# Optimization experiments

Measured on AMD Instinct MI355X. Metric: run time of the kernel, lower is better.

The kernel has to match this reference:

```python
import jax, jax.numpy as jnp
import numpy as np

B, S, D, H = 4, 2048, 256, 4
HD = D // H          # head_dim = 64
SPARSITY = 0.1
NH2 = H * H          # 16, distill feature size


def _linear_params(key, out_d, in_d):
    # torch nn.Linear default init: U(-1/sqrt(in), 1/sqrt(in)) for W and b
    limit = 1.0 / np.sqrt(in_d)
    kw, kb = jax.random.split(key)
    W = jax.random.uniform(kw, (out_d, in_d), minval=-limit, maxval=limit, dtype=jnp.float32)
    b = jax.random.uniform(kb, (out_d,), minval=-limit, maxval=limit, dtype=jnp.float32)
    return W, b


def setup_inputs() -> dict:
    key = jax.random.key(0)
    ks = jax.random.split(key, 8)
    x = jax.random.normal(ks[0], (B, S, D), dtype=jnp.float32)
    Wq, bq = _linear_params(ks[1], D, D)
    Wk, bk = _linear_params(ks[2], D, D)
    Wv, bv = _linear_params(ks[3], D, D)
    Wd, bd = _linear_params(ks[4], NH2, NH2)      # distill: 16 -> 16
    Wg, bg = _linear_params(ks[5], NH2, D)        # gate: dim -> 16 (then sigmoid)
    Wgp, bgp = _linear_params(ks[6], D, NH2)      # gate_projection: 16 -> dim
    Wo, bo = _linear_params(ks[7], D, D)          # out: dim -> dim
    return dict(x=x, Wq=Wq, bq=bq, Wk=Wk, bk=bk, Wv=Wv, bv=bv,
                Wd=Wd, bd=bd, Wg=Wg, bg=bg, Wgp=Wgp, bgp=bgp, Wo=Wo, bo=bo)


def reference(x, Wq, bq, Wk, bk, Wv, bv, Wd, bd, Wg, bg, Wgp, bgp, Wo, bo):
    b, s, d = x.shape
    scale = HD ** -0.5
    # QKV projections, split into heads: [b, h, s, hd]
    Q = (x @ Wq.T + bq).reshape(b, s, H, HD).transpose(0, 2, 1, 3)
    K = (x @ Wk.T + bk).reshape(b, s, H, HD).transpose(0, 2, 1, 3)
    V = (x @ Wv.T + bv).reshape(b, s, H, HD).transpose(0, 2, 1, 3)
    scores = jnp.einsum('bhqd,bhkd->bhqk', Q, K) * scale  # [b,h,s,s]
    # per-row quantile threshold (torch.quantile linear interpolation == jnp default)
    q = 1.0 - SPARSITY  # 0.9
    thr = jnp.quantile(scores, q, axis=-1, keepdims=True)
    masked = jnp.where(scores >= thr, scores, -jnp.inf)
    probs = jax.nn.softmax(masked, axis=-1)
    att = jnp.einsum('bhqk,bhkd->bhqd', probs, V)
    att = att.transpose(0, 2, 1, 3).reshape(b, s, d)  # [b,s,dim]
    # distill: view as (-1, 16) -> Linear(16,16) -> view back
    distilled = (att.reshape(-1, NH2) @ Wd.T + bd).reshape(b, s, d)
    # gate from mean-pooled input
    g = jax.nn.sigmoid(x.mean(axis=1) @ Wg.T + bg)  # [b,16]
    g = (g @ Wgp.T + bgp)[:, None, :]               # [b,1,dim] broadcast over seq
    mixed = g * distilled + (1.0 - g) * att
    return mixed @ Wo.T + bo
```

## Files before the change

### kernel.cpp

```cpp
#include <hip/hip_runtime.h>
#include <hip/hip_bf16.h>
#include <math.h>


#define CAP 128

typedef __attribute__((ext_vector_type(8))) short short8;
typedef __attribute__((ext_vector_type(4))) float floatx4;
typedef _Float16 half8 __attribute__((ext_vector_type(8)));
typedef _Float16 half4v __attribute__((ext_vector_type(4)));
#define MFMA16(a,b,c) __builtin_amdgcn_mfma_f32_16x16x32_bf16(a,b,c,0,0,0)
#define MFMAH(a,b,c)  __builtin_amdgcn_mfma_f32_16x16x32_f16(a,b,c,0,0,0)

__device__ __forceinline__ float umt(unsigned u){
  return __uint_as_float((u & 0x80000000u) ? (u & 0x7fffffffu) : ~u);
}
__device__ __forceinline__ float wmin_f(float v){
  #pragma unroll
  for (int m=1;m<64;m<<=1) v = fminf(v, __shfl_xor(v,m,64));
  return v;
}
__device__ __forceinline__ int mbcnt64(unsigned long long m){
  return (int)__builtin_amdgcn_mbcnt_hi((unsigned)(m>>32),
         __builtin_amdgcn_mbcnt_lo((unsigned)(m & 0xffffffffull), 0u));
}
__device__ __forceinline__ short8 ldb8(const __hip_bfloat16* p){
  return *(const short8*)p;
}

#define FULLSEL(SU, PSTART, V206, V205)                                        \
  {                                                                            \
    unsigned v = (PSTART);                                                     \
    _Pragma("unroll 1")                                                        \
    for (int bit = 19; bit >= 0; --bit){                                       \
      const float cf = umt(v | (1u << bit));                                   \
      int n = 0;                                                               \
      _Pragma("unroll")                                                        \
      for (int i = 0; i < 32; i++) n += (int)__popcll(__ballot(SU[i] >= cf));  \
      if (n >= 206) v |= (1u << bit);                                          \
    }                                                                          \
    V206 = umt(v);                                                             \
    int cgt = 0; float mn = 3.0e38f;                                           \
    _Pragma("unroll")                                                          \
    for (int i = 0; i < 32; i++){                                              \
      const float u = SU[i];                                                   \
      const bool gt = (u > V206);                                              \
      cgt += (int)__popcll(__ballot(gt));                                      \
      mn = (gt && u < mn) ? u : mn;                                            \
    }                                                                          \
    mn = wmin_f(mn);                                                           \
    V205 = (cgt == 205) ? mn : V206;                                           \
  }

__global__ void xpart_kernel(const float* __restrict__ x, float* __restrict__ xpart,
                             __hip_bfloat16* __restrict__ xh, __hip_bfloat16* __restrict__ xl){
  const int ch = blockIdx.x, b = blockIdx.y, t = threadIdx.x;
  const size_t base = ((size_t)b*2048 + (size_t)ch*16)*256 + t;
  float s = 0.f;
  #pragma unroll
  for (int i=0;i<16;i++){
    const float v = x[base + (size_t)i*256];
    s += v;
    const __hip_bfloat16 h = __float2bfloat16(v);
    xh[base + (size_t)i*256] = h;
    xl[base + (size_t)i*256] = __float2bfloat16(v - __bfloat162float(h));
  }
  xpart[(size_t)(b*128+ch)*256 + t] = s;
}

__global__ void wconv_kernel(const float* __restrict__ Wq, const float* __restrict__ Wk,
                             const float* __restrict__ Wv, const float* __restrict__ Wo,
                             __hip_bfloat16* __restrict__ wh, __hip_bfloat16* __restrict__ wl){
  const int mat = blockIdx.x >> 6;
  const float* W = (mat==0) ? Wq : (mat==1) ? Wk : (mat==2) ? Wv : Wo;
  const int off = (blockIdx.x & 63)*1024 + threadIdx.x*4;
  const float4 v = *(const float4*)&W[off];
  const float vv[4] = {v.x, v.y, v.z, v.w};
  short hs[4], ls[4];
  #pragma unroll
  for (int i=0;i<4;i++){
    const __hip_bfloat16 h = __float2bfloat16(vv[i]);
    const __hip_bfloat16 l = __float2bfloat16(vv[i] - __bfloat162float(h));
    hs[i] = *(const short*)&h; ls[i] = *(const short*)&l;
  }
  const size_t o = (size_t)mat*65536 + off;
  *(short4*)((short*)wh + o) = make_short4(hs[0],hs[1],hs[2],hs[3]);
  *(short4*)((short*)wl + o) = make_short4(ls[0],ls[1],ls[2],ls[3]);
}

__global__ void gate_kernel(const float* __restrict__ xpart,
                            const float* __restrict__ Wg, const float* __restrict__ bg,
                            const float* __restrict__ Wgp,const float* __restrict__ bgp,
                            float* __restrict__ gate_ws){
  __shared__ float xm[256];
  __shared__ float part[16][17];
  __shared__ float g16[16];
  const int t = threadIdx.x;
  const int b = blockIdx.x;
  float s = 0.f;
  for (int ch=0; ch<128; ch++) s += xpart[(size_t)(b*128+ch)*256 + t];
  xm[t] = s * (1.0f/2048.0f);
  __syncthreads();
  {
    const int j = t >> 4, dg = t & 15;
    float p = 0.f;
    #pragma unroll
    for (int d=0; d<16; d++) p = fmaf(xm[dg*16+d], Wg[j*256 + dg*16 + d], p);
    part[j][dg] = p;
  }
  __syncthreads();
  if (t < 16){
    float z = bg[t];
    #pragma unroll
    for (int g=0; g<16; g++) z += part[t][g];
    g16[t] = 1.0f/(1.0f + __expf(-z));
  }
  __syncthreads();
  float z2 = bgp[t];
  #pragma unroll
  for (int j=0;j<16;j++) z2 = fmaf(g16[j], Wgp[t*16+j], z2);
  gate_ws[b*256 + t] = z2;
}

__global__ __launch_bounds__(256) void qkv_gemm(
    const __hip_bfloat16* __restrict__ xh, const __hip_bfloat16* __restrict__ xl,
    const __hip_bfloat16* __restrict__ wh, const __hip_bfloat16* __restrict__ wl,
    const float* __restrict__ bq, const float* __restrict__ bk, const float* __restrict__ bv,
    __hip_bfloat16* __restrict__ qh, __hip_bfloat16* __restrict__ ql,
    __hip_bfloat16* __restrict__ kh, __hip_bfloat16* __restrict__ kl,
    _Float16* __restrict__ vth, _Float16* __restrict__ vtl){
  __shared__ short Ah[64][40], Al[64][40];
  __shared__ short Bh[64][40], Bl[64][40];
  const int m0 = blockIdx.x * 64;
  const int n0g = blockIdx.y * 64;
  const int sect = n0g >> 8;
  const int nl0 = n0g & 255;
  const __hip_bfloat16* Wh = wh + (size_t)sect*65536;
  const __hip_bfloat16* Wl = wl + (size_t)sect*65536;
  const float* bias = (sect==0) ? bq : ((sect==1) ? bk : bv);
  const int tid = threadIdx.x;
  const int lr = tid >> 2, lc = tid & 3;
  const int w = tid >> 6, ln = tid & 63;
  const int lm = ln & 15, lk = (ln >> 4) * 8;

  floatx4 acc[4];
  #pragma unroll
  for (int tl=0;tl<4;tl++) acc[tl] = (floatx4){0.f,0.f,0.f,0.f};

  for (int k0 = 0; k0 < 256; k0 += 32){
    const short8 a_h = ldb8(xh + (size_t)(m0 +lr)*256 + k0 + lc*8);
    const short8 a_l = ldb8(xl + (size_t)(m0 +lr)*256 + k0 + lc*8);
    const short8 b_h = ldb8(Wh + (size_t)(nl0+lr)*256 + k0 + lc*8);
    const short8 b_l = ldb8(Wl + (size_t)(nl0+lr)*256 + k0 + lc*8);
    __syncthreads();
    *(short8*)&Ah[lr][lc*8] = a_h;
    *(short8*)&Al[lr][lc*8] = a_l;
    *(short8*)&Bh[lr][lc*8] = b_h;
    *(short8*)&Bl[lr][lc*8] = b_l;
    __syncthreads();
    const short8 ah8 = *(const short8*)&Ah[w*16+lm][lk];
    const short8 al8 = *(const short8*)&Al[w*16+lm][lk];
    #pragma unroll
    for (int tl = 0; tl < 4; tl++){
      const short8 bh8 = *(const short8*)&Bh[tl*16+lm][lk];
      const short8 bl8 = *(const short8*)&Bl[tl*16+lm][lk];
      acc[tl] = MFMA16(ah8, bh8, acc[tl]);
      acc[tl] = MFMA16(al8, bh8, acc[tl]);
      acc[tl] = MFMA16(ah8, bl8, acc[tl]);
      acc[tl] = MFMA16(al8, bl8, acc[tl]);
    }
  }

  #pragma unroll
  for (int tl = 0; tl < 4; tl++){
    const int f = nl0 + tl*16 + lm;
    const int hh = f >> 6, hd = f & 63;
    const float bf = bias[f];
    if (sect == 2){
      const int mB = m0 + w*16 + (ln >> 4)*4;
      const int bidx = mB >> 11, s0 = mB & 2047;
      half4v hv, lv;
      #pragma unroll
      for (int i=0;i<4;i++){
        const float val = acc[tl][i] + bf;
        const _Float16 hx = (_Float16)val;
        hv[i] = hx;
        lv[i] = (_Float16)(val - (float)hx);
      }
      const size_t row = (size_t)((bidx*4+hh)*64 + hd);
      *(half4v*)(vth + row*2048 + s0) = hv;
      *(half4v*)(vtl + row*2048 + s0) = lv;
    } else {
      #pragma unroll
      for (int i=0;i<4;i++){
        const int m = m0 + w*16 + (ln >> 4)*4 + i;
        const int bidx = m >> 11, s = m & 2047;
        const float val = acc[tl][i] + bf;
        const size_t idx = (size_t)((bidx*4+hh)*2048 + s)*64 + hd;
        const __hip_bfloat16 hi = __float2bfloat16(val);
        const float lo = val - __bfloat162float(hi);
        if (sect == 0){ qh[idx] = hi; ql[idx] = __float2bfloat16(lo); }
        else          { kh[idx] = hi; kl[idx] = __float2bfloat16(lo); }
      }
    }
  }
}

__global__ __launch_bounds__(512, 4) void attn_kernel(
    const __hip_bfloat16* __restrict__ qh, const __hip_bfloat16* __restrict__ ql,
    const __hip_bfloat16* __restrict__ kh, const __hip_bfloat16* __restrict__ kl,
    const _Float16* __restrict__ vth, const _Float16* __restrict__ vtl,
    const float* __restrict__ Wd, const float* __restrict__ bd,
    const float* __restrict__ gate_ws,
    __hip_bfloat16* __restrict__ mixh, __hip_bfloat16* __restrict__ mixl){
  __shared__ __align__(16) char smem[70336];
  float (*buf0)[516] = (float (*)[516])smem;
  float (*buf1)[516] = (float (*)[516])(smem + 33024);
  float (*obuf)[66] = (float (*)[66])(smem + 66048);
  float* zbuf = (float*)(smem + 70272);

  const int bh = blockIdx.y;
  const int q0 = blockIdx.x * 16;
  const int tid = threadIdx.x;
  const int w = tid >> 6, ln = tid & 63;
  const int lm = ln & 15;
  const int lk = (ln >> 4) * 8;
  const int qa = 2*w, qb = 2*w + 1;

  const __hip_bfloat16* Qh = qh + ((size_t)bh*2048 + q0)*64;
  const __hip_bfloat16* Ql = ql + ((size_t)bh*2048 + q0)*64;
  const __hip_bfloat16* Kh = kh + ((size_t)bh*2048 + w*256)*64;
  const __hip_bfloat16* Kl = kl + ((size_t)bh*2048 + w*256)*64;

  float su0[32], su1[32];

  const short8 ah0 = ldb8(Qh + lm*64 + lk);
  const short8 ah1 = ldb8(Qh + lm*64 + 32 + lk);
  const short8 al0 = ldb8(Ql + lm*64 + lk);
  const short8 al1 = ldb8(Ql + lm*64 + 32 + lk);

  #pragma unroll
  for (int c = 0; c < 4; c++){
    float (*bufc)[516] = (c & 1) ? buf1 : buf0;
    floatx4 acc[4];
    #pragma unroll
    for (int tl = 0; tl < 4; tl++){
      const int krow = c*64 + tl*16 + lm;
      short8 bh0 = ldb8(Kh + krow*64 + lk);
      short8 bh1 = ldb8(Kh + krow*64 + 32 + lk);
      short8 bl0 = ldb8(Kl + krow*64 + lk);
      short8 bl1 = ldb8(Kl + krow*64 + 32 + lk);
      floatx4 a = {0.f,0.f,0.f,0.f};
      a = MFMA16(ah0, bh0, a);
      a = MFMA16(ah1, bh1, a);
      a = MFMA16(al0, bh0, a);
      a = MFMA16(al1, bh1, a);
      a = MFMA16(ah0, bl0, a);
      a = MFMA16(ah1, bl1, a);
      a = MFMA16(al0, bl0, a);
      a = MFMA16(al1, bl1, a);
      acc[tl] = a;
    }
    const int wr = (ln >> 4) * 4;
    #pragma unroll
    for (int tl = 0; tl < 4; tl++){
      const int col = w*64 + tl*16 + lm;
      bufc[wr+0][col] = acc[tl].x * 0.125f;
      bufc[wr+1][col] = acc[tl].y * 0.125f;
      bufc[wr+2][col] = acc[tl].z * 0.125f;
      bufc[wr+3][col] = acc[tl].w * 0.125f;
    }
    __syncthreads();
    float4 ra0 = *(const float4*)&bufc[qa][4*ln];
    float4 ra1 = *(const float4*)&bufc[qa][256 + 4*ln];
    float4 rb0 = *(const float4*)&bufc[qb][4*ln];
    float4 rb1 = *(const float4*)&bufc[qb][256 + 4*ln];
    const int o = c*8;
    su0[o+0]=ra0.x; su0[o+1]=ra0.y; su0[o+2]=ra0.z; su0[o+3]=ra0.w;
    su0[o+4]=ra1.x; su0[o+5]=ra1.y; su0[o+6]=ra1.z; su0[o+7]=ra1.w;
    su1[o+0]=rb0.x; su1[o+1]=rb0.y; su1[o+2]=rb0.z; su1[o+3]=rb0.w;
    su1[o+4]=rb1.x; su1[o+5]=rb1.y; su1[o+6]=rb1.z; su1[o+7]=rb1.w;
  }
  __syncthreads();

  unsigned p0 = 0, p1 = 0;
  #pragma unroll 1
  for (int bit = 31; bit >= 20; --bit){
    const float c0f = umt(p0 | (1u << bit));
    const float c1f = umt(p1 | (1u << bit));
    int v0 = 0, n1 = 0;
    #pragma unroll
    for (int i = 0; i < 32; i++){
      v0 += (su0[i] >= c0f) ? 1 : 0;
      n1 += (int)__popcll(__ballot(su1[i] >= c1f));
    }
    #pragma unroll
    for (int m=1;m<64;m<<=1) v0 += __shfl_xor(v0,m,64);
    p0 |= (v0 >= 206) ? (1u << bit) : 0u;
    if (n1 >= 206) p1 |= (1u << bit);
  }

  const int b = bh >> 2, h = bh & 3;

  const float pf0  = umt(p0),             pf1  = umt(p1);
  const float hif0 = umt(p0 + 0x100000u), hif1 = umt(p1 + 0x100000u);
  float* cand0 = (float*)(smem + 33024 + (size_t)w*1024);
  float* cand1 = (float*)(smem + 33024 + (size_t)w*1024 + 512);

  int above0 = 0, nc0 = 0, above1 = 0, nc1 = 0;
  float mx0 = -3.0e38f, mx1 = -3.0e38f, mnab0 = 3.0e38f, mnab1 = 3.0e38f;
  #pragma unroll
  for (int i = 0; i < 32; i++){
    const float u0 = su0[i], u1 = su1[i];
    mx0 = fmaxf(mx0, u0);
    mx1 = fmaxf(mx1, u1);
    const bool ab0 = (u0 >= hif0), ab1 = (u1 >= hif1);
    above0 += ab0 ? 1 : 0;
    above1 += ab1 ? 1 : 0;
    if (ab0) mnab0 = fminf(mnab0, u0);
    if (ab1) mnab1 = fminf(mnab1, u1);
    const bool cd0 = (u0 >= pf0) && !ab0, cd1 = (u1 >= pf1) && !ab1;
    const unsigned long long bal0 = __ballot(cd0);
    if (cd0){
      const int pos = nc0 + mbcnt64(bal0);
      if (pos < CAP) cand0[pos] = u0;
    }
    nc0 += (int)__popcll(bal0);
    const unsigned long long bal1 = __ballot(cd1);
    if (cd1){
      const int pos = nc1 + mbcnt64(bal1);
      if (pos < CAP) cand1[pos] = u1;
    }
    nc1 += (int)__popcll(bal1);
  }
  int ab01 = above0 | (above1 << 16);
  #pragma unroll
  for (int m=1;m<64;m<<=1){
    ab01  += __shfl_xor(ab01, m,64);
    mx0   = fmaxf(mx0,   __shfl_xor(mx0,  m,64));
    mx1   = fmaxf(mx1,   __shfl_xor(mx1,  m,64));
    mnab0 = fminf(mnab0, __shfl_xor(mnab0,m,64));
    mnab1 = fminf(mnab1, __shfl_xor(mnab1,m,64));
  }
  above0 = ab01 & 0xffff;
  above1 = ab01 >> 16;

  float v206_0, v205_0, v206_1, v205_1;
  if (__builtin_expect(nc0 <= CAP && nc1 <= CAP, 1)){
    const int j0 = 206 - above0, j1 = 206 - above1;
    const float cv00 = (ln      < nc0) ? cand0[ln]      : -3.0e38f;
    const float cv01 = (ln + 64 < nc0) ? cand0[ln + 64] : -3.0e38f;
    const float cv10 = (ln      < nc1) ? cand1[ln]      : -3.0e38f;
    const float cv11 = (ln + 64 < nc1) ? cand1[ln + 64] : -3.0e38f;
    unsigned v0 = p0, v1 = p1;
    #pragma unroll 1
    for (int bit = 19; bit >= 0; --bit){
      const float cf0 = umt(v0 | (1u << bit));
      const float cf1 = umt(v1 | (1u << bit));
      const int n0 = (int)__popcll(__ballot(cv00 >= cf0))
                   + (int)__popcll(__ballot(cv01 >= cf0));
      const int n1 = (int)__popcll(__ballot(cv10 >= cf1))
                   + (int)__popcll(__ballot(cv11 >= cf1));
      if (n0 >= j0) v0 |= (1u << bit);
      if (n1 >= j1) v1 |= (1u << bit);
    }
    v206_0 = umt(v0);
    v206_1 = umt(v1);
    const int cgtc0 = (int)__popcll(__ballot(cv00 > v206_0))
                    + (int)__popcll(__ballot(cv01 > v206_0));
    const int cgtc1 = (int)__popcll(__ballot(cv10 > v206_1))
                    + (int)__popcll(__ballot(cv11 > v206_1));
    float mnc0 = 3.0e38f, mnc1 = 3.0e38f;
    if (cv00 > v206_0) mnc0 = fminf(mnc0, cv00);
    if (cv01 > v206_0) mnc0 = fminf(mnc0, cv01);
    if (cv10 > v206_1) mnc1 = fminf(mnc1, cv10);
    if (cv11 > v206_1) mnc1 = fminf(mnc1, cv11);
    #pragma unroll
    for (int m=1;m<64;m<<=1){
      mnc0 = fminf(mnc0, __shfl_xor(mnc0,m,64));
      mnc1 = fminf(mnc1, __shfl_xor(mnc1,m,64));
    }
    const int cgt0 = above0 + cgtc0, cgt1 = above1 + cgtc1;
    v205_0 = (cgt0 == 205) ? ((cgtc0 > 0) ? mnc0 : mnab0) : v206_0;
    v205_1 = (cgt1 == 205) ? ((cgtc1 > 0) ? mnc1 : mnab1) : v206_1;
  } else {
    FULLSEL(su0, p0, v206_0, v205_0);
    FULLSEL(su1, p1, v206_1, v205_1);
  }

  const float thr0 = (float)((double)v206_0 + 0.3*((double)v205_0 - (double)v206_0));
  const float thr1 = (float)((double)v206_1 + 0.3*((double)v205_1 - (double)v206_1));

  float zl0 = 0.f, zl1 = 0.f;
  char* rba = smem + (size_t)qa*2048 + ((size_t)(ln >> 4) << 9)
            + (size_t)((((ln & 15) << 3)) ^ ((qa & 7) << 4));
  char* rbb = smem + (size_t)qb*2048 + ((size_t)(ln >> 4) << 9)
            + (size_t)((((ln & 15) << 3)) ^ ((qb & 7) << 4));

  const int ct = w & 3, khq = w >> 2;
  const int arow = ln & 15;
  const int sw = (arow & 7) << 4;
  const char* prow = smem + (size_t)arow*2048;
  const int klog0 = (khq << 10) + ((ln >> 4) << 4);
  floatx4 acch = {0.f,0.f,0.f,0.f};
  floatx4 accl = {0.f,0.f,0.f,0.f};

  #pragma unroll
  for (int hp = 0; hp < 2; hp++){
    #pragma unroll
    for (int c = 0; c < 4; c++){
      half4v pk0, pk1;
      #pragma unroll
      for (int jj = 0; jj < 4; jj++){
        const int i = c*8 + hp*4 + jj;
        const float s0 = su0[i], s1 = su1[i];
        const float pr0 = (s0 >= thr0) ? __expf(s0 - mx0) : 0.f;
        const float pr1 = (s1 >= thr1) ? __expf(s1 - mx1) : 0.f;
        const _Float16 ph0 = (_Float16)pr0;
        const _Float16 ph1 = (_Float16)pr1;
        zl0 += (float)ph0;
        zl1 += (float)ph1;
        pk0[jj] = ph0;
        pk1[jj] = ph1;
      }
      *(half4v*)(rba + c*128) = pk0;
      *(half4v*)(rbb + c*128) = pk1;
    }
    if (hp == 1){
      #pragma unroll
      for (int m=1;m<64;m<<=1){
        zl0 += __shfl_xor(zl0,m,64);
        zl1 += __shfl_xor(zl1,m,64);
      }
      if (ln == 0){ zbuf[qa] = 1.0f / zl0; zbuf[qb] = 1.0f / zl1; }
    }
    __syncthreads();

    const _Float16* vhp_ = vth + ((size_t)bh*64 + ct*16 + arow)*2048
                         + (hp << 10) + (khq << 9) + ((ln >> 4) << 3);
    const _Float16* vlp_ = vtl + ((size_t)bh*64 + ct*16 + arow)*2048
                         + (hp << 10) + (khq << 9) + ((ln >> 4) << 3);
    #pragma unroll 4
    for (int kk = 0; kk < 16; kk++){
      const half8 a   = *(const half8*)(prow + ((klog0 + kk*64) ^ sw));
      const half8 vh8 = *(const half8*)(vhp_ + kk*32);
      const half8 vl8 = *(const half8*)(vlp_ + kk*32);
      acch = MFMAH(a, vh8, acch);
      accl = MFMAH(a, vl8, accl);
    }
    if (hp == 0) __syncthreads();
  }
  floatx4 acc = acch + accl;

  float gt = 0.f, bda = 0.f;
  float wdv[16];
  if (khq == 1){
    const int r0 = (ln >> 4) * 4;
    #pragma unroll
    for (int i = 0; i < 4; i++) obuf[r0+i][ct*16 + arow] = acc[i];
  } else {
    gt  = gate_ws[(size_t)b*256 + h*64 + ct*16 + arow];
    bda = bd[arow];
    #pragma unroll
    for (int m4 = 0; m4 < 4; m4++){
      const float4 t4 = *(const float4*)&Wd[arow*16 + m4*4];
      wdv[m4*4+0]=t4.x; wdv[m4*4+1]=t4.y; wdv[m4*4+2]=t4.z; wdv[m4*4+3]=t4.w;
    }
  }
  __syncthreads();
  if (khq == 0){
    const int r0 = (ln >> 4) * 4;
    const int gb = ln & 48;
    #pragma unroll
    for (int i = 0; i < 4; i++){
      const int r = r0 + i;
      const float o = (acc[i] + obuf[r][ct*16 + arow]) * zbuf[r];
      float d = bda;
      #pragma unroll
      for (int m = 0; m < 16; m++)
        d = fmaf(__shfl(o, gb + m, 64), wdv[m], d);
      const float mixed = gt*d + (1.0f - gt)*o;
      const size_t oidx = (size_t)(b*2048 + q0 + r)*256 + h*64 + ct*16 + arow;
      const __hip_bfloat16 mhv = __float2bfloat16(mixed);
      mixh[oidx] = mhv;
      mixl[oidx] = __float2bfloat16(mixed - __bfloat162float(mhv));
    }
  }
}

__global__ __launch_bounds__(256) void out_gemm(
    const __hip_bfloat16* __restrict__ mh, const __hip_bfloat16* __restrict__ ml,
    const __hip_bfloat16* __restrict__ wh, const __hip_bfloat16* __restrict__ wl,
    const float* __restrict__ bo, float* __restrict__ out){
  __shared__ short Ah[64][40], Al[64][40];
  __shared__ short Bh[64][40], Bl[64][40];
  const int m0 = blockIdx.x * 64;
  const int n0 = blockIdx.y * 64;
  const __hip_bfloat16* Wh = wh + (size_t)3*65536;
  const __hip_bfloat16* Wl = wl + (size_t)3*65536;
  const int tid = threadIdx.x;
  const int lr = tid >> 2, lc = tid & 3;
  const int w = tid >> 6, ln = tid & 63;
  const int lm = ln & 15, lk = (ln >> 4) * 8;

  floatx4 acc[4];
  #pragma unroll
  for (int tl=0;tl<4;tl++) acc[tl] = (floatx4){0.f,0.f,0.f,0.f};

  for (int k0 = 0; k0 < 256; k0 += 32){
    const short8 a_h = ldb8(mh + (size_t)(m0+lr)*256 + k0 + lc*8);
    const short8 a_l = ldb8(ml + (size_t)(m0+lr)*256 + k0 + lc*8);
    const short8 b_h = ldb8(Wh + (size_t)(n0+lr)*256 + k0 + lc*8);
    const short8 b_l = ldb8(Wl + (size_t)(n0+lr)*256 + k0 + lc*8);
    __syncthreads();
    *(short8*)&Ah[lr][lc*8] = a_h;
    *(short8*)&Al[lr][lc*8] = a_l;
    *(short8*)&Bh[lr][lc*8] = b_h;
    *(short8*)&Bl[lr][lc*8] = b_l;
    __syncthreads();
    const short8 ah8 = *(const short8*)&Ah[w*16+lm][lk];
    const short8 al8 = *(const short8*)&Al[w*16+lm][lk];
    #pragma unroll
    for (int tl = 0; tl < 4; tl++){
      const short8 bh8 = *(const short8*)&Bh[tl*16+lm][lk];
      const short8 bl8 = *(const short8*)&Bl[tl*16+lm][lk];
      acc[tl] = MFMA16(ah8, bh8, acc[tl]);
      acc[tl] = MFMA16(al8, bh8, acc[tl]);
      acc[tl] = MFMA16(ah8, bl8, acc[tl]);
      acc[tl] = MFMA16(al8, bl8, acc[tl]);
    }
  }

  #pragma unroll
  for (int tl = 0; tl < 4; tl++){
    const int f = n0 + tl*16 + lm;
    const float bf = bo[f];
    #pragma unroll
    for (int i=0;i<4;i++){
      const int m = m0 + w*16 + (ln >> 4)*4 + i;
      out[(size_t)m*256 + f] = acc[tl][i] + bf;
    }
  }
}

extern "C" void kernel_launch(void* const* d_in, const int* in_sizes, int n_in,
                              void* d_out, int out_size, void* d_ws, size_t ws_size,
                              hipStream_t stream) {
  const float* x   = (const float*)d_in[0];
  const float* Wq  = (const float*)d_in[1];  const float* bq  = (const float*)d_in[2];
  const float* Wk  = (const float*)d_in[3];  const float* bk  = (const float*)d_in[4];
  const float* Wv  = (const float*)d_in[5];  const float* bv  = (const float*)d_in[6];
  const float* Wd  = (const float*)d_in[7];  const float* bd  = (const float*)d_in[8];
  const float* Wg  = (const float*)d_in[9];  const float* bg  = (const float*)d_in[10];
  const float* Wgp = (const float*)d_in[11]; const float* bgp = (const float*)d_in[12];
  const float* Wo  = (const float*)d_in[13]; const float* bo  = (const float*)d_in[14];

  char* base = (char*)d_ws;
  __hip_bfloat16* mixh = (__hip_bfloat16*)(base);
  __hip_bfloat16* mixl = (__hip_bfloat16*)(base + (size_t)( 4<<20));
  __hip_bfloat16* qh = (__hip_bfloat16*)(base + (size_t)( 8<<20));
  __hip_bfloat16* ql = (__hip_bfloat16*)(base + (size_t)(12<<20));
  __hip_bfloat16* kh = (__hip_bfloat16*)(base + (size_t)(16<<20));
  __hip_bfloat16* kl = (__hip_bfloat16*)(base + (size_t)(20<<20));
  _Float16* vth = (_Float16*)(base + (size_t)(24<<20));
  _Float16* vtl = (_Float16*)(base + (size_t)(28<<20));
  __hip_bfloat16* xh = (__hip_bfloat16*)(base + (size_t)(32<<20));
  __hip_bfloat16* xl = (__hip_bfloat16*)(base + (size_t)(36<<20));
  __hip_bfloat16* wh = (__hip_bfloat16*)(base + (size_t)(40<<20));
  __hip_bfloat16* wl = (__hip_bfloat16*)(base + (size_t)(40<<20) + (512<<10));
  float* xpart  = (float*)(base + (size_t)(41<<20));
  float* gate_ws= (float*)(base + (size_t)(41<<20) + (512<<10));

  xpart_kernel<<<dim3(128,4), 256, 0, stream>>>(x, xpart, xh, xl);
  wconv_kernel<<<256, 256, 0, stream>>>(Wq, Wk, Wv, Wo, wh, wl);
  gate_kernel<<<4, 256, 0, stream>>>(xpart, Wg, bg, Wgp, bgp, gate_ws);
  qkv_gemm<<<dim3(128,12), 256, 0, stream>>>(xh, xl, wh, wl, bq, bk, bv,
                                             qh, ql, kh, kl, vth, vtl);
  attn_kernel<<<dim3(128,16), 512, 0, stream>>>(qh, ql, kh, kl, vth, vtl,
                                                Wd, bd, gate_ws, mixh, mixl);
  out_gemm<<<dim3(128,4), 256, 0, stream>>>(mixh, mixl, wh, wl, bo, (float*)d_out);
}
```

Before: 397.0 us.

## Bracket quantile candidates with mean/std window instead of 12-bit radix prefix

Replaces the 12-iteration radix prefix pass over all 2048 scores per row with a single mean/variance reduction, then keeps candidates in the window [mean+sd, mean+1.5sd) for the exact bitwise selection. The candidate cap doubles to 256 and the fine selection now scans all 32 bits over four registers per lane. If the window does not bracket the 206th value or overflows, it falls back to a full 32-bit radix select over every score. This relies on near-Gaussian score distributions; heavy-tailed rows would take the slower fallback more often.

After: 380.8 us. 4.1% less time.

```diff
diff --git a/kernel.cpp b/kernel.cpp
--- a/kernel.cpp
+++ b/kernel.cpp
@@ -3,7 +3,7 @@
 #include <math.h>
 
 
-#define CAP 128
+#define CAP 256
 
 typedef __attribute__((ext_vector_type(8))) short short8;
 typedef __attribute__((ext_vector_type(4))) float floatx4;
@@ -28,11 +28,11 @@
   return *(const short8*)p;
 }
 
-#define FULLSEL(SU, PSTART, V206, V205)                                        \
+#define FULLSEL(SU, V206, V205)                                                \
   {                                                                            \
-    unsigned v = (PSTART);                                                     \
+    unsigned v = 0u;                                                           \
     _Pragma("unroll 1")                                                        \
-    for (int bit = 19; bit >= 0; --bit){                                       \
+    for (int bit = 31; bit >= 0; --bit){                                       \
       const float cf = umt(v | (1u << bit));                                   \
       int n = 0;                                                               \
       _Pragma("unroll")                                                        \
@@ -283,43 +283,44 @@
   }
   __syncthreads();
 
-  unsigned p0 = 0, p1 = 0;
-  #pragma unroll 1
-  for (int bit = 31; bit >= 20; --bit){
-    const float c0f = umt(p0 | (1u << bit));
-    const float c1f = umt(p1 | (1u << bit));
-    int v0 = 0, n1 = 0;
-    #pragma unroll
-    for (int i = 0; i < 32; i++){
-      v0 += (su0[i] >= c0f) ? 1 : 0;
-      n1 += (int)__popcll(__ballot(su1[i] >= c1f));
-    }
-    #pragma unroll
-    for (int m=1;m<64;m<<=1) v0 += __shfl_xor(v0,m,64);
-    p0 |= (v0 >= 206) ? (1u << bit) : 0u;
-    if (n1 >= 206) p1 |= (1u << bit);
-  }
-
-  const int b = bh >> 2, h = bh & 3;
-
-  const float pf0  = umt(p0),             pf1  = umt(p1);
-  const float hif0 = umt(p0 + 0x100000u), hif1 = umt(p1 + 0x100000u);
-  float* cand0 = (float*)(smem + 33024 + (size_t)w*1024);
-  float* cand1 = (float*)(smem + 33024 + (size_t)w*1024 + 512);
-
-  int above0 = 0, nc0 = 0, above1 = 0, nc1 = 0;
-  float mx0 = -3.0e38f, mx1 = -3.0e38f, mnab0 = 3.0e38f, mnab1 = 3.0e38f;
+  float sm0 = 0.f, sm1 = 0.f, sq0 = 0.f, sq1 = 0.f;
+  float mx0 = -3.0e38f, mx1 = -3.0e38f;
   #pragma unroll
   for (int i = 0; i < 32; i++){
     const float u0 = su0[i], u1 = su1[i];
-    mx0 = fmaxf(mx0, u0);
-    mx1 = fmaxf(mx1, u1);
-    const bool ab0 = (u0 >= hif0), ab1 = (u1 >= hif1);
+    sm0 += u0; sm1 += u1;
+    sq0 = fmaf(u0, u0, sq0); sq1 = fmaf(u1, u1, sq1);
+    mx0 = fmaxf(mx0, u0); mx1 = fmaxf(mx1, u1);
+  }
+  #pragma unroll
+  for (int m=1;m<64;m<<=1){
+    sm0 += __shfl_xor(sm0,m,64); sm1 += __shfl_xor(sm1,m,64);
+    sq0 += __shfl_xor(sq0,m,64); sq1 += __shfl_xor(sq1,m,64);
+    mx0 = fmaxf(mx0, __shfl_xor(mx0,m,64));
+    mx1 = fmaxf(mx1, __shfl_xor(mx1,m,64));
+  }
+  const float mean0 = sm0 * (1.f/2048.f), mean1 = sm1 * (1.f/2048.f);
+  const float sd0 = sqrtf(fmaxf(sq0*(1.f/2048.f) - mean0*mean0, 0.f));
+  const float sd1 = sqrtf(fmaxf(sq1*(1.f/2048.f) - mean1*mean1, 0.f));
+  const float lo0 = mean0 + sd0, lo1 = mean1 + sd1;
+  const float hi0 = fmaf(1.5f, sd0, mean0), hi1 = fmaf(1.5f, sd1, mean1);
+
+  const int b = bh >> 2, h = bh & 3;
+
+  float* cand0 = (float*)(smem + 33024 + (size_t)w*2048);
+  float* cand1 = (float*)(smem + 33024 + (size_t)w*2048 + 1024);
+
+  int above0 = 0, nc0 = 0, above1 = 0, nc1 = 0;
+  float mnab0 = 3.0e38f, mnab1 = 3.0e38f;
+  #pragma unroll
+  for (int i = 0; i < 32; i++){
+    const float u0 = su0[i], u1 = su1[i];
+    const bool ab0 = (u0 >= hi0), ab1 = (u1 >= hi1);
     above0 += ab0 ? 1 : 0;
     above1 += ab1 ? 1 : 0;
     if (ab0) mnab0 = fminf(mnab0, u0);
     if (ab1) mnab1 = fminf(mnab1, u1);
-    const bool cd0 = (u0 >= pf0) && !ab0, cd1 = (u1 >= pf1) && !ab1;
+    const bool cd0 = (u0 >= lo0) && !ab0, cd1 = (u1 >= lo1) && !ab1;
     const unsigned long long bal0 = __ballot(cd0);
     if (cd0){
       const int pos = nc0 + mbcnt64(bal0);
@@ -337,44 +338,61 @@
   #pragma unroll
   for (int m=1;m<64;m<<=1){
     ab01  += __shfl_xor(ab01, m,64);
-    mx0   = fmaxf(mx0,   __shfl_xor(mx0,  m,64));
-    mx1   = fmaxf(mx1,   __shfl_xor(mx1,  m,64));
     mnab0 = fminf(mnab0, __shfl_xor(mnab0,m,64));
     mnab1 = fminf(mnab1, __shfl_xor(mnab1,m,64));
   }
   above0 = ab01 & 0xffff;
   above1 = ab01 >> 16;
 
+  const bool vld0 = (above0 < 206) && (above0 + nc0 >= 206) && (nc0 <= CAP);
+  const bool vld1 = (above1 < 206) && (above1 + nc1 >= 206) && (nc1 <= CAP);
+
   float v206_0, v205_0, v206_1, v205_1;
-  if (__builtin_expect(nc0 <= CAP && nc1 <= CAP, 1)){
+  if (__builtin_expect(vld0 && vld1, 1)){
     const int j0 = 206 - above0, j1 = 206 - above1;
-    const float cv00 = (ln      < nc0) ? cand0[ln]      : -3.0e38f;
-    const float cv01 = (ln + 64 < nc0) ? cand0[ln + 64] : -3.0e38f;
-    const float cv10 = (ln      < nc1) ? cand1[ln]      : -3.0e38f;
-    const float cv11 = (ln + 64 < nc1) ? cand1[ln + 64] : -3.0e38f;
-    unsigned v0 = p0, v1 = p1;
+    const float cv00 = (ln       < nc0) ? cand0[ln]       : -3.0e38f;
+    const float cv01 = (ln + 64  < nc0) ? cand0[ln + 64]  : -3.0e38f;
+    const float cv02 = (ln + 128 < nc0) ? cand0[ln + 128] : -3.0e38f;
+    const float cv03 = (ln + 192 < nc0) ? cand0[ln + 192] : -3.0e38f;
+    const float cv10 = (ln       < nc1) ? cand1[ln]       : -3.0e38f;
+    const float cv11 = (ln + 64  < nc1) ? cand1[ln + 64]  : -3.0e38f;
+    const float cv12 = (ln + 128 < nc1) ? cand1[ln + 128] : -3.0e38f;
+    const float cv13 = (ln + 192 < nc1) ? cand1[ln + 192] : -3.0e38f;
+    unsigned v0 = 0u, v1 = 0u;
     #pragma unroll 1
-    for (int bit = 19; bit >= 0; --bit){
+    for (int bit = 31; bit >= 0; --bit){
       const float cf0 = umt(v0 | (1u << bit));
       const float cf1 = umt(v1 | (1u << bit));
       const int n0 = (int)__popcll(__ballot(cv00 >= cf0))
-                   + (int)__popcll(__ballot(cv01 >= cf0));
+                   + (int)__popcll(__ballot(cv01 >= cf0))
+                   + (int)__popcll(__ballot(cv02 >= cf0))
+                   + (int)__popcll(__ballot(cv03 >= cf0));
       const int n1 = (int)__popcll(__ballot(cv10 >= cf1))
-                   + (int)__popcll(__ballot(cv11 >= cf1));
+                   + (int)__popcll(__ballot(cv11 >= cf1))
+                   + (int)__popcll(__ballot(cv12 >= cf1))
+                   + (int)__popcll(__ballot(cv13 >= cf1));
       if (n0 >= j0) v0 |= (1u << bit);
       if (n1 >= j1) v1 |= (1u << bit);
     }
     v206_0 = umt(v0);
     v206_1 = umt(v1);
     const int cgtc0 = (int)__popcll(__ballot(cv00 > v206_0))
-                    + (int)__popcll(__ballot(cv01 > v206_0));
+                    + (int)__popcll(__ballot(cv01 > v206_0))
+                    + (int)__popcll(__ballot(cv02 > v206_0))
+                    + (int)__popcll(__ballot(cv03 > v206_0));
     const int cgtc1 = (int)__popcll(__ballot(cv10 > v206_1))
-                    + (int)__popcll(__ballot(cv11 > v206_1));
+                    + (int)__popcll(__ballot(cv11 > v206_1))
+                    + (int)__popcll(__ballot(cv12 > v206_1))
+                    + (int)__popcll(__ballot(cv13 > v206_1));
     float mnc0 = 3.0e38f, mnc1 = 3.0e38f;
     if (cv00 > v206_0) mnc0 = fminf(mnc0, cv00);
     if (cv01 > v206_0) mnc0 = fminf(mnc0, cv01);
+    if (cv02 > v206_0) mnc0 = fminf(mnc0, cv02);
+    if (cv03 > v206_0) mnc0 = fminf(mnc0, cv03);
     if (cv10 > v206_1) mnc1 = fminf(mnc1, cv10);
     if (cv11 > v206_1) mnc1 = fminf(mnc1, cv11);
+    if (cv12 > v206_1) mnc1 = fminf(mnc1, cv12);
+    if (cv13 > v206_1) mnc1 = fminf(mnc1, cv13);
     #pragma unroll
     for (int m=1;m<64;m<<=1){
       mnc0 = fminf(mnc0, __shfl_xor(mnc0,m,64));
@@ -384,8 +402,8 @@
     v205_0 = (cgt0 == 205) ? ((cgtc0 > 0) ? mnc0 : mnab0) : v206_0;
     v205_1 = (cgt1 == 205) ? ((cgtc1 > 0) ? mnc1 : mnab1) : v206_1;
   } else {
-    FULLSEL(su0, p0, v206_0, v205_0);
-    FULLSEL(su1, p1, v206_1, v205_1);
+    FULLSEL(su0, v206_0, v205_0);
+    FULLSEL(su1, v206_1, v205_1);
   }
 
   const float thr0 = (float)((double)v206_0 + 0.3*((double)v205_0 - (double)v206_0));
```
